# Performance work log

Hardware: AMD Instinct MI355X
Metric: run time of the kernel (lower is better)

Reference implementation:

```python
import jax, jax.numpy as jnp
import numpy as np

B, G, N = 32, 512, 512          # batch, group (POMO rollouts), problem size
EMB, H, DK = 128, 8, 16          # embedding_dim, head_num, qkv_dim (H*DK == EMB)
E, FH, K = 8, 512, 2             # num_experts, ff_hidden_dim, top-k
SQRT_EMB = 11.313708498984761    # sqrt(128), model_params['sqrt_embedding_dim']
CLIP = 10.0                      # logit_clipping


def setup_inputs() -> dict:
    key = jax.random.key(0)
    ks = jax.random.split(key, 22)
    s = 0.05
    d = {}
    d["pref"] = jax.random.uniform(ks[0], (2,), dtype=jnp.float32)
    d["graph"] = jax.random.normal(ks[1], (B, 1, EMB), dtype=jnp.float32)
    d["capacity"] = jax.random.uniform(ks[2], (B, G), dtype=jnp.float32)
    d["encoded_nodes"] = jax.random.normal(ks[3], (B, N, EMB), dtype=jnp.float32)
    d["ninf_mask"] = jnp.zeros((B, G, N), dtype=jnp.float32)
    # hyper-network MLP (note: original has NO activations between hyper_fc layers)
    d["fc1_w"] = jax.random.normal(ks[4], (256, 2)) * s
    d["fc1_b"] = jax.random.normal(ks[5], (256,)) * s
    d["fc2_w"] = jax.random.normal(ks[6], (256, 256)) * s
    d["fc2_b"] = jax.random.normal(ks[7], (256,)) * s
    d["fc3_w"] = jax.random.normal(ks[8], (8, 256)) * s
    d["fc3_b"] = jax.random.normal(ks[9], (8,)) * s
    # hyper heads producing the attention weight matrices (Linear(embd_dim=2, out), no bias)
    d["hWq"] = jax.random.normal(ks[10], ((1 + EMB) * H * DK, 2)) * 0.02
    d["hWk"] = jax.random.normal(ks[11], (EMB * H * DK, 2)) * 0.02
    d["hWv"] = jax.random.normal(ks[12], (EMB * H * DK, 2)) * 0.02
    d["hWc"] = jax.random.normal(ks[13], (EMB * H * DK, 2)) * 0.02
    # MoE combine layer: gating (token input + 8-dim pref embedding) and E expert MLPs
    d["gate_w"] = jax.random.normal(ks[14], (H * DK, E)) * s
    d["gate_pref_w"] = jax.random.normal(ks[15], (8, E)) * s
    d["e_w1"] = jax.random.normal(ks[16], (E, FH, H * DK)) * (1.0 / np.sqrt(H * DK))
    d["e_b1"] = jnp.zeros((E, FH), dtype=jnp.float32)
    d["e_w2"] = jax.random.normal(ks[17], (E, EMB, FH)) * (1.0 / np.sqrt(FH))
    d["e_b2"] = jnp.zeros((E, EMB), dtype=jnp.float32)
    d = {k2: v.astype(jnp.float32) for k2, v in d.items()}
    return d


def _heads(x):  # [B, n, H*DK] -> [B, H, n, DK]
    b, n, _ = x.shape
    return x.reshape(b, n, H, DK).transpose(0, 2, 1, 3)


def reference(pref, graph, capacity, encoded_nodes, ninf_mask,
              fc1_w, fc1_b, fc2_w, fc2_b, fc3_w, fc3_b,
              hWq, hWk, hWv, hWc,
              gate_w, gate_pref_w, e_w1, e_b1, e_w2, e_b2):
    # ---- assign(pref): hypernet generates attention weight matrices ----
    h = fc1_w @ pref + fc1_b
    h = fc2_w @ h + fc2_b
    mid = fc3_w @ h + fc3_b                      # [8] == mid_embd_pref
    Wq = (hWq @ mid[0:2]).reshape(H * DK, 1 + EMB)
    Wk = (hWk @ mid[2:4]).reshape(H * DK, EMB)
    Wv = (hWv @ mid[4:6]).reshape(H * DK, EMB)
    Wc = (hWc @ mid[6:8]).reshape(H * DK, EMB)
    # ---- set_kv ----
    k = _heads(encoded_nodes @ Wk.T)             # [B,H,N,DK]
    v = _heads(encoded_nodes @ Wv.T)
    # ---- forward ----
    inp = jnp.concatenate(
        [jnp.broadcast_to(graph, (B, G, EMB)), capacity[:, :, None]], axis=2)
    q = _heads(inp @ Wq.T)                       # [B,H,G,DK]
    score = jnp.einsum('bhgd,bhnd->bhgn', q, k) / jnp.sqrt(jnp.float32(DK))
    score = score + ninf_mask[:, None, :, :]
    attn = jax.nn.softmax(score, axis=3)
    out = jnp.einsum('bhgn,bhnd->bhgd', attn, v)
    out = out.transpose(0, 2, 1, 3).reshape(B, G, H * DK)   # [B,G,128]
    # ---- MoE combine (noisy top-k gating, deterministic at inference) ----
    logits = out @ gate_w + mid @ gate_pref_w    # [B,G,E]
    vals, idx = jax.lax.top_k(logits, K)
    gv = jax.nn.softmax(vals, axis=-1)           # softmax over selected k (T=1)
    gates = jnp.sum(jax.nn.one_hot(idx, E, dtype=out.dtype) * gv[..., None], axis=-2)
    hdn = jax.nn.relu(jnp.einsum('bgi,ehi->bgeh', out, e_w1) + e_b1)
    y = jnp.einsum('bgeh,eoh->bgeo', hdn, e_w2) + e_b2
    moe_out = jnp.einsum('bgeo,bge->bgo', y, gates)          # [B,G,EMB]
    # ---- combine + tanh-clipped masked softmax over nodes ----
    mh = moe_out @ Wc.T                           # [B,G,EMB]
    sc = jnp.einsum('bge,bne->bgn', mh, encoded_nodes) / SQRT_EMB
    probs = jax.nn.softmax(CLIP * jnp.tanh(sc) + ninf_mask, axis=2)
    return probs
```

## Files before the change

### kernel.cpp

```cpp
#include <hip/hip_runtime.h>


typedef __attribute__((ext_vector_type(8))) __bf16 bf16x8;
typedef __attribute__((ext_vector_type(4))) float f32x4;

static constexpr long OFF_MID   = 0;
static constexpr long OFF_PREFL = 8;
static constexpr long OFF_WL    = 16;
static constexpr long OFF_WKB   = 256;
static constexpr long OFF_WVB   = 8448;
static constexpr long OFF_WCB   = 16640;
static constexpr long OFF_QB    = 24832;
static constexpr long OFF_MFLAG = 28928;
static constexpr long OFF_CNT   = 33024;
static constexpr long OFF_TOK   = 33032;
static constexpr long OFF_WGT   = 164104;
static constexpr long OFF_AO    = 295176;
static constexpr long OFF_Y0    = 1343752;
static constexpr long OFF_Y1    = 2392328;
static constexpr long OFF_ENCB  = 3440904;

__device__ __forceinline__ unsigned f2bf(float x) {
  union { float f; unsigned u; } v; v.f = x;
  return ((v.u + 0x7FFFu + ((v.u >> 16) & 1u)) >> 16) & 0xFFFFu;
}
__device__ __forceinline__ float bflo(unsigned u) {
  union { unsigned u; float f; } v; v.u = u << 16; return v.f;
}
__device__ __forceinline__ float bfhi(unsigned u) {
  union { unsigned u; float f; } v; v.u = u & 0xFFFF0000u; return v.f;
}

__global__ __launch_bounds__(256)
void k_prep1(const float* __restrict__ pref, const float* __restrict__ fc1w,
             const float* __restrict__ fc1b, const float* __restrict__ fc2w,
             const float* __restrict__ fc2b, const float* __restrict__ fc3w,
             const float* __restrict__ fc3b, const float* __restrict__ gpw,
             const float* __restrict__ hWq, const float* __restrict__ mask,
             const float* __restrict__ ew1, const float* __restrict__ ew2,
             const float* __restrict__ enc,
             unsigned short* __restrict__ w1b, unsigned short* __restrict__ w2b,
             unsigned short* __restrict__ encb, float* __restrict__ ws) {
  const int bid = blockIdx.x;
  const int tid = threadIdx.x;
  if (bid == 0) {
    __shared__ float h1[256];
    __shared__ float h2[256];
    __shared__ float mid[8];
    const float p0 = pref[0], p1 = pref[1];
    h1[tid] = fc1w[2*tid]*p0 + fc1w[2*tid+1]*p1 + fc1b[tid];
    __syncthreads();
    float s = 0.f;
    for (int j = 0; j < 256; ++j) s = fmaf(fc2w[tid*256+j], h1[j], s);
    h2[tid] = s + fc2b[tid];
    __syncthreads();
    if (tid < 8) {
      float s2 = 0.f;
      for (int j = 0; j < 256; ++j) s2 = fmaf(fc3w[tid*256+j], h2[j], s2);
      mid[tid] = s2 + fc3b[tid];
    }
    __syncthreads();
    if (tid < 8) {
      ws[OFF_MID + tid] = mid[tid];
      float s3 = 0.f;
      for (int i = 0; i < 8; ++i) s3 = fmaf(mid[i], gpw[i*8 + tid], s3);
      ws[OFF_PREFL + tid] = s3;
      ((int*)(ws + OFF_CNT))[tid] = 0;
    }
    if (tid >= 16 && tid < 144) {
      const int o = tid - 16;
      ws[OFF_WL + o] = hWq[((long)o*129 + 128)*2]*mid[0]
                     + hWq[((long)o*129 + 128)*2 + 1]*mid[1];
    }
    return;
  }
  if (bid <= 3072) {
    const int i = (bid-1)*256 + tid;
    const float* src;
    unsigned short* dst;
    if (i < 131072)      { src = ew1 + (long)i*4;          dst = w1b + (long)i*4; }
    else if (i < 262144) { src = ew2 + (long)(i-131072)*4; dst = w2b + (long)(i-131072)*4; }
    else                 { src = enc + (long)(i-262144)*4; dst = encb + (long)(i-262144)*4; }
    const float4 v = *(const float4*)src;
    uint2 p;
    p.x = f2bf(v.x) | (f2bf(v.y) << 16);
    p.y = f2bf(v.z) | (f2bf(v.w) << 16);
    *(uint2*)dst = p;
    return;
  }
  __shared__ int fl[8];
  const int rowbase = (bid - 3073) * 8;
  const int r = tid >> 5, seg = tid & 31;
  if (tid < 8) fl[tid] = 0;
  __syncthreads();
  const float* mrow = mask + (long)(rowbase + r)*512 + seg*16;
  int nz = 0;
#pragma unroll
  for (int c = 0; c < 4; ++c) {
    const float4 v = *(const float4*)(mrow + c*4);
    nz |= (v.x != 0.f) | (v.y != 0.f) | (v.z != 0.f) | (v.w != 0.f);
  }
  if (nz) atomicOr(&fl[r], 1);
  __syncthreads();
  if (tid < 8) ((char*)(ws + OFF_MFLAG))[rowbase + tid] = (char)fl[tid];
}

__global__ __launch_bounds__(256)
void k_prep2(const float* __restrict__ graph,
             const float* __restrict__ hWq, const float* __restrict__ hWk,
             const float* __restrict__ hWv, const float* __restrict__ hWc,
             float* __restrict__ ws) {
  const int bid = blockIdx.x;
  const int tid = threadIdx.x;
  __shared__ float mid[8];
  __shared__ float g[2][128];
  if (tid < 8) mid[tid] = ws[OFF_MID + tid];
  __syncthreads();
  if (bid < 192) {
    const int i = bid*256 + tid;
    if (i < 16384) {
      ((unsigned short*)(ws + OFF_WKB))[i] =
          (unsigned short)f2bf(hWk[2*i]*mid[2] + hWk[2*i+1]*mid[3]);
    } else if (i < 32768) {
      const int j = i - 16384;
      ((unsigned short*)(ws + OFF_WVB))[j] =
          (unsigned short)f2bf(hWv[2*j]*mid[4] + hWv[2*j+1]*mid[5]);
    } else {
      const int j = i - 32768;
      ((unsigned short*)(ws + OFF_WCB))[j] =
          (unsigned short)f2bf(hWc[2*j]*mid[6] + hWc[2*j+1]*mid[7]);
    }
    return;
  }
  const int qb = bid - 192;
  const int b0 = qb*2;
  {
    const int bb = tid >> 7, ii = tid & 127;
    g[bb][ii] = graph[(b0+bb)*128 + ii];
  }
  __syncthreads();
  const float m0 = mid[0], m1 = mid[1];
  const int bb = tid >> 7, o = tid & 127;
  const float* hq = hWq + (long)o*129*2;
  float acc = 0.f;
  for (int i2 = 0; i2 < 128; ++i2) {
    const float w = hq[2*i2]*m0 + hq[2*i2+1]*m1;
    acc = fmaf(g[bb][i2], w, acc);
  }
  ws[OFF_QB + (b0+bb)*128 + o] = acc;
}

__device__ __forceinline__ bf16x8 ld_frag(const unsigned short* base, int row, int bytecol) {
  const int addr = row*256 + (bytecol ^ ((row & 7) << 4));
  return *(const bf16x8*)((const char*)base + addr);
}

__global__ __launch_bounds__(256)
void k_kv(const unsigned short* __restrict__ encb,
          const unsigned short* __restrict__ wkb,
          const unsigned short* __restrict__ wvb,
          unsigned short* __restrict__ Kb, unsigned short* __restrict__ Vtg) {
  __shared__ unsigned short Ws[128*128];
  __shared__ unsigned short Xs[64*128];
  const int tid = threadIdx.x;
  const int nbase = blockIdx.x * 64;
  const unsigned short* Wb = blockIdx.y ? wvb : wkb;
#pragma unroll
  for (int s = 0; s < 8; ++s) {
    const int id = tid + s*256;
    const int fr = id >> 4, c16 = id & 15;
    const uint4 v = *(const uint4*)(Wb + (long)fr*128 + c16*8);
    *(uint4*)((char*)Ws + fr*256 + ((c16*16) ^ ((fr & 7) << 4))) = v;
  }
#pragma unroll
  for (int s = 0; s < 4; ++s) {
    const int id = tid + s*256;
    const int r = id >> 4, c16 = id & 15;
    const uint4 v = *(const uint4*)(encb + (long)(nbase + r)*128 + c16*8);
    *(uint4*)((char*)Xs + r*256 + ((c16*16) ^ ((r & 7) << 4))) = v;
  }
  __syncthreads();
  const int w = tid >> 6, l = tid & 63, lq = l >> 4, lr = l & 15;
  f32x4 acc[2][4];
#pragma unroll
  for (int a = 0; a < 2; ++a)
#pragma unroll
    for (int m = 0; m < 4; ++m) acc[a][m] = (f32x4){0.f, 0.f, 0.f, 0.f};
#pragma unroll
  for (int ks = 0; ks < 4; ++ks) {
    const int bcol = ks*64 + lq*16;
    const bf16x8 a0 = ld_frag(Ws, (2*w  )*16 + lr, bcol);
    const bf16x8 a1 = ld_frag(Ws, (2*w+1)*16 + lr, bcol);
    const bf16x8 b0 = ld_frag(Xs, 0*16 + lr, bcol);
    const bf16x8 b1 = ld_frag(Xs, 1*16 + lr, bcol);
    const bf16x8 b2 = ld_frag(Xs, 2*16 + lr, bcol);
    const bf16x8 b3 = ld_frag(Xs, 3*16 + lr, bcol);
    acc[0][0] = __builtin_amdgcn_mfma_f32_16x16x32_bf16(a0, b0, acc[0][0], 0, 0, 0);
    acc[0][1] = __builtin_amdgcn_mfma_f32_16x16x32_bf16(a0, b1, acc[0][1], 0, 0, 0);
    acc[0][2] = __builtin_amdgcn_mfma_f32_16x16x32_bf16(a0, b2, acc[0][2], 0, 0, 0);
    acc[0][3] = __builtin_amdgcn_mfma_f32_16x16x32_bf16(a0, b3, acc[0][3], 0, 0, 0);
    acc[1][0] = __builtin_amdgcn_mfma_f32_16x16x32_bf16(a1, b0, acc[1][0], 0, 0, 0);
    acc[1][1] = __builtin_amdgcn_mfma_f32_16x16x32_bf16(a1, b1, acc[1][1], 0, 0, 0);
    acc[1][2] = __builtin_amdgcn_mfma_f32_16x16x32_bf16(a1, b2, acc[1][2], 0, 0, 0);
    acc[1][3] = __builtin_amdgcn_mfma_f32_16x16x32_bf16(a1, b3, acc[1][3], 0, 0, 0);
  }
  if (blockIdx.y == 0) {
#pragma unroll
    for (int obi = 0; obi < 2; ++obi) {
      const int o0 = (2*w + obi)*16 + lq*4;
#pragma unroll
      for (int mb = 0; mb < 4; ++mb) {
        const long n = nbase + mb*16 + lr;
        uint2 pp;
        pp.x = f2bf(acc[obi][mb][0]) | (f2bf(acc[obi][mb][1]) << 16);
        pp.y = f2bf(acc[obi][mb][2]) | (f2bf(acc[obi][mb][3]) << 16);
        *(uint2*)(Kb + n*128 + o0) = pp;
      }
    }
  } else {
    const int b = nbase >> 9;
    const int nn0 = nbase & 511;
#pragma unroll
    for (int obi = 0; obi < 2; ++obi) {
      const int o0 = (2*w + obi)*16 + lq*4;
#pragma unroll
      for (int mb = 0; mb < 4; ++mb) {
        const int nn = nn0 + mb*16 + lr;
#pragma unroll
        for (int j = 0; j < 4; ++j) {
          const int o = o0 + j;
          Vtg[(((long)b*8 + (o >> 4))*16 + (o & 15))*512 + nn] =
              (unsigned short)f2bf(acc[obi][mb][j]);
        }
      }
    }
  }
}

__global__ __launch_bounds__(512, 8)
void k_attn(const unsigned short* __restrict__ Kb,
            const unsigned short* __restrict__ Vtg,
            const float* __restrict__ ws, const float* __restrict__ cap,
            const float* __restrict__ mask, unsigned short* __restrict__ AOb) {
  const int bid = blockIdx.x;
  const int b = bid & 31, h = (bid >> 5) & 7, qh = bid >> 8;
  __shared__ unsigned short Kbf[512*24];
  __shared__ unsigned short Vt[16*536];
  __shared__ unsigned short Ps[8*16*40];
  const int tid = threadIdx.x;
#pragma unroll
  for (int it = 0; it < 2; ++it) {
    const int i = tid + it*512;
    const int n = i >> 1, hf = i & 1;
    const uint4 kv = *(const uint4*)(Kb + (long)(b*512 + n)*128 + h*16 + hf*8);
    *(uint4*)(Kbf + n*24 + hf*8) = kv;
    const int d = i >> 6, c = i & 63;
    const uint4 vv = *(const uint4*)(Vtg + ((long)(b*8 + h)*16 + d)*512 + c*8);
    *(uint4*)(Vt + d*536 + c*8) = vv;
  }
  const int w = tid >> 6, l = tid & 63;
  const int lq = l >> 4, lr = l & 15;
  const int grow = qh*128 + w*16 + lr;
  bf16x8 qf;
  {
    union { uint4 u; bf16x8 v; } cv;
    cv.u = make_uint4(0u, 0u, 0u, 0u);
    if (lq < 2) {
      const float* qbp = ws + OFF_QB + b*128 + h*16 + lq*8;
      const float* wlp = ws + OFF_WL + h*16 + lq*8;
      const float cp = cap[b*512 + grow];
      float qv[8];
#pragma unroll
      for (int j = 0; j < 8; ++j) qv[j] = (qbp[j] + cp*wlp[j]) * 0.25f;
      cv.u.x = f2bf(qv[0]) | (f2bf(qv[1]) << 16);
      cv.u.y = f2bf(qv[2]) | (f2bf(qv[3]) << 16);
      cv.u.z = f2bf(qv[4]) | (f2bf(qv[5]) << 16);
      cv.u.w = f2bf(qv[6]) | (f2bf(qv[7]) << 16);
    }
    qf = cv.v;
  }
  const int mf = ((const char*)(ws + OFF_MFLAG))[b*512 + grow];
  const bool usemask = __any(mf != 0);
  unsigned short* Pw = Ps + w*16*40;
  const int psw = (lr & 3) << 3;
  __syncthreads();
  float lsum = 0.f;
  f32x4 oaccA = {0.f, 0.f, 0.f, 0.f};
  f32x4 oaccB = {0.f, 0.f, 0.f, 0.f};
  const float* mrow = mask + ((long)(b*512 + grow))*512 + lq*4;
#pragma unroll 2
  for (int qc = 0; qc < 16; ++qc) {
    const int n0 = qc*32;
    f32x4 s[2];
#pragma unroll
    for (int nb = 0; nb < 2; ++nb) {
      bf16x8 kf;
      {
        union { uint4 u; bf16x8 v; } cv;
        cv.u = make_uint4(0u, 0u, 0u, 0u);
        if (lq < 2) cv.u = *(const uint4*)(Kbf + (n0 + nb*16 + lr)*24 + lq*8);
        kf = cv.v;
      }
      s[nb] = __builtin_amdgcn_mfma_f32_16x16x32_bf16(
          kf, qf, (f32x4){0.f, 0.f, 0.f, 0.f}, 0, 0, 0);
      if (usemask) {
        const float4 mk = *(const float4*)(mrow + n0 + nb*16);
        s[nb][0] += mk.x; s[nb][1] += mk.y; s[nb][2] += mk.z; s[nb][3] += mk.w;
      }
    }
#pragma unroll
    for (int nb = 0; nb < 2; ++nb) {
      const float e0 = __expf(s[nb][0]);
      const float e1 = __expf(s[nb][1]);
      const float e2 = __expf(s[nb][2]);
      const float e3 = __expf(s[nb][3]);
      lsum += (e0 + e1) + (e2 + e3);
      uint2 pp;
      asm("v_cvt_pk_bf16_f32 %0, %1, %2" : "=v"(pp.x) : "v"(e0), "v"(e1));
      asm("v_cvt_pk_bf16_f32 %0, %1, %2" : "=v"(pp.y) : "v"(e2), "v"(e3));
      *(uint2*)(Pw + lr*40 + ((nb*16 + lq*4) ^ psw)) = pp;
    }
    const bf16x8 va = *(const bf16x8*)(Vt + lr*536 + n0 + lq*8);
    const bf16x8 pb = *(const bf16x8*)(Pw + lr*40 + (lq*8 ^ psw));
    if (qc & 1) oaccB = __builtin_amdgcn_mfma_f32_16x16x32_bf16(va, pb, oaccB, 0, 0, 0);
    else        oaccA = __builtin_amdgcn_mfma_f32_16x16x32_bf16(va, pb, oaccA, 0, 0, 0);
  }
  lsum += __shfl_xor(lsum, 16);
  lsum += __shfl_xor(lsum, 32);
  const float inv = 1.f / lsum;
  uint2 op;
  op.x = f2bf((oaccA[0]+oaccB[0])*inv) | (f2bf((oaccA[1]+oaccB[1])*inv) << 16);
  op.y = f2bf((oaccA[2]+oaccB[2])*inv) | (f2bf((oaccA[3]+oaccB[3])*inv) << 16);
  *(uint2*)(AOb + (long)(b*512 + grow)*128 + h*16 + lq*4) = op;
}

__global__ __launch_bounds__(256)
void k_gate(const unsigned short* __restrict__ AOb, const float* __restrict__ gw,
            float* __restrict__ ws) {
  const int tid = threadIdx.x;
  const int t = blockIdx.x*256 + tid;
  const unsigned short* x = AOb + (long)t*128;
  float lg[8];
  {
    const float* pl = ws + OFF_PREFL;
#pragma unroll
    for (int e = 0; e < 8; ++e) lg[e] = pl[e];
  }
  for (int i = 0; i < 128; i += 8) {
    const uint4 xv = *(const uint4*)(x + i);
    float xf[8];
    xf[0] = bflo(xv.x); xf[1] = bfhi(xv.x);
    xf[2] = bflo(xv.y); xf[3] = bfhi(xv.y);
    xf[4] = bflo(xv.z); xf[5] = bfhi(xv.z);
    xf[6] = bflo(xv.w); xf[7] = bfhi(xv.w);
#pragma unroll
    for (int u = 0; u < 8; ++u) {
      const float xi = xf[u];
      const float4 ga = *(const float4*)(gw + (i+u)*8);
      const float4 gb = *(const float4*)(gw + (i+u)*8 + 4);
      lg[0] = fmaf(xi, ga.x, lg[0]); lg[1] = fmaf(xi, ga.y, lg[1]);
      lg[2] = fmaf(xi, ga.z, lg[2]); lg[3] = fmaf(xi, ga.w, lg[3]);
      lg[4] = fmaf(xi, gb.x, lg[4]); lg[5] = fmaf(xi, gb.y, lg[5]);
      lg[6] = fmaf(xi, gb.z, lg[6]); lg[7] = fmaf(xi, gb.w, lg[7]);
    }
  }
  int i0 = 0; float v0 = lg[0];
#pragma unroll
  for (int e = 1; e < 8; ++e) if (lg[e] > v0) { v0 = lg[e]; i0 = e; }
  int i1 = -1; float v1 = -1e30f;
#pragma unroll
  for (int e = 0; e < 8; ++e) if (e != i0 && lg[e] > v1) { v1 = lg[e]; i1 = e; }
  const float e1 = __expf(v1 - v0);
  const float w0 = 1.f / (1.f + e1);
  const float w1 = 1.f - w0;
  __shared__ int bcnt[8];
  __shared__ int gbase[8];
  if (tid < 8) bcnt[tid] = 0;
  __syncthreads();
  const int p0 = atomicAdd(&bcnt[i0], 1);
  const int p1 = atomicAdd(&bcnt[i1], 1);
  __syncthreads();
  if (tid < 8) {
    int* cnt = (int*)(ws + OFF_CNT);
    gbase[tid] = (bcnt[tid] > 0) ? atomicAdd(&cnt[tid], bcnt[tid]) : 0;
  }
  __syncthreads();
  int* tokp = (int*)(ws + OFF_TOK);
  float* wgtp = ws + OFF_WGT;
  const int s0 = gbase[i0] + p0;
  tokp[i0*16384 + s0] = t;
  wgtp[i0*16384 + s0] = w0;
  const int s1 = gbase[i1] + p1;
  tokp[i1*16384 + s1] = t | (1 << 30);
  wgtp[i1*16384 + s1] = w1;
}

__global__ __launch_bounds__(256)
void k_moe(const unsigned short* __restrict__ AOb,
           const unsigned short* __restrict__ w1b,
           const unsigned short* __restrict__ w2b,
           const float* __restrict__ eb1, const float* __restrict__ eb2,
           float* __restrict__ ws,
           unsigned short* __restrict__ Y0b, unsigned short* __restrict__ Y1b) {
  const int e = blockIdx.y;
  const int ce = ((const int*)(ws + OFF_CNT))[e];
  const int base = blockIdx.x * 64;
  if (base >= ce) return;
  const int nt = min(64, ce - base);

  __shared__ unsigned short Xs[64*128];
  __shared__ unsigned short Wts[128*128];
  __shared__ unsigned short Hs[64*128];
  __shared__ float seb1[512];
  __shared__ float seb2[128];
  __shared__ int   stok[64];
  __shared__ float swgt[64];

  const int tid = threadIdx.x;
  if (tid < 64) {
    if (tid < nt) {
      stok[tid] = ((const int*)(ws + OFF_TOK))[e*16384 + base + tid];
      swgt[tid] = (ws + OFF_WGT)[e*16384 + base + tid];
    } else { stok[tid] = -1; swgt[tid] = 0.f; }
  }
  for (int i = tid; i < 512; i += 256) seb1[i] = eb1[e*512 + i];
  if (tid < 128) seb2[tid] = eb2[e*128 + tid];
  __syncthreads();

#pragma unroll
  for (int r4 = 0; r4 < 4; ++r4) {
    const int id = tid + r4*256;
    const int r = id >> 4, c16 = id & 15;
    const int pk = stok[r];
    uint4 v = make_uint4(0u, 0u, 0u, 0u);
    if (pk >= 0) v = *(const uint4*)(AOb + (long)(pk & 0x3FFFFFFF)*128 + c16*8);
    *(uint4*)((char*)Xs + r*256 + ((c16*16) ^ ((r & 7) << 4))) = v;
  }

  const int w  = tid >> 6;
  const int l  = tid & 63;
  const int lq = l >> 4;
  const int lr = l & 15;

  f32x4 yacc[2][4];
#pragma unroll
  for (int a = 0; a < 2; ++a)
#pragma unroll
    for (int m = 0; m < 4; ++m) yacc[a][m] = (f32x4){0.f, 0.f, 0.f, 0.f};

  for (int fc = 0; fc < 4; ++fc) {
    __syncthreads();
    {
      const long wb = (long)(e*512 + fc*128) * 128;
#pragma unroll
      for (int s = 0; s < 8; ++s) {
        const int id = tid + s*256;
        const int fr = id >> 4, c16 = id & 15;
        const uint4 v = *(const uint4*)(w1b + wb + (long)fr*128 + c16*8);
        *(uint4*)((char*)Wts + fr*256 + ((c16*16) ^ ((fr & 7) << 4))) = v;
      }
    }
    __syncthreads();
    f32x4 hacc[2][4];
#pragma unroll
    for (int a = 0; a < 2; ++a)
#pragma unroll
      for (int m = 0; m < 4; ++m) hacc[a][m] = (f32x4){0.f, 0.f, 0.f, 0.f};
#pragma unroll
    for (int ks = 0; ks < 4; ++ks) {
      const int bcol = ks*64 + lq*16;
      const bf16x8 a0 = ld_frag(Wts, (2*w  )*16 + lr, bcol);
      const bf16x8 a1 = ld_frag(Wts, (2*w+1)*16 + lr, bcol);
      const bf16x8 b0 = ld_frag(Xs,  0*16 + lr, bcol);
      const bf16x8 b1 = ld_frag(Xs,  1*16 + lr, bcol);
      const bf16x8 b2 = ld_frag(Xs,  2*16 + lr, bcol);
      const bf16x8 b3 = ld_frag(Xs,  3*16 + lr, bcol);
      hacc[0][0] = __builtin_amdgcn_mfma_f32_16x16x32_bf16(a0, b0, hacc[0][0], 0, 0, 0);
      hacc[0][1] = __builtin_amdgcn_mfma_f32_16x16x32_bf16(a0, b1, hacc[0][1], 0, 0, 0);
      hacc[0][2] = __builtin_amdgcn_mfma_f32_16x16x32_bf16(a0, b2, hacc[0][2], 0, 0, 0);
      hacc[0][3] = __builtin_amdgcn_mfma_f32_16x16x32_bf16(a0, b3, hacc[0][3], 0, 0, 0);
      hacc[1][0] = __builtin_amdgcn_mfma_f32_16x16x32_bf16(a1, b0, hacc[1][0], 0, 0, 0);
      hacc[1][1] = __builtin_amdgcn_mfma_f32_16x16x32_bf16(a1, b1, hacc[1][1], 0, 0, 0);
      hacc[1][2] = __builtin_amdgcn_mfma_f32_16x16x32_bf16(a1, b2, hacc[1][2], 0, 0, 0);
      hacc[1][3] = __builtin_amdgcn_mfma_f32_16x16x32_bf16(a1, b3, hacc[1][3], 0, 0, 0);
    }
    __syncthreads();
#pragma unroll
    for (int fbi = 0; fbi < 2; ++fbi) {
      const int fb = (2*w + fbi)*16 + lq*4;
      const float4 bia = *(const float4*)&seb1[fc*128 + fb];
#pragma unroll
      for (int mb = 0; mb < 4; ++mb) {
        const int m = mb*16 + lr;
        const float h0 = fmaxf(hacc[fbi][mb][0] + bia.x, 0.f);
        const float h1 = fmaxf(hacc[fbi][mb][1] + bia.y, 0.f);
        const float h2 = fmaxf(hacc[fbi][mb][2] + bia.z, 0.f);
        const float h3 = fmaxf(hacc[fbi][mb][3] + bia.w, 0.f);
        uint2 p;
        p.x = f2bf(h0) | (f2bf(h1) << 16);
        p.y = f2bf(h2) | (f2bf(h3) << 16);
        const int bc = (fb*2) ^ ((m & 7) << 4);
        *(uint2*)((char*)Hs + m*256 + bc) = p;
      }
    }
    {
      const long wb = (long)(e*128) * 512 + fc*128;
#pragma unroll
      for (int s = 0; s < 8; ++s) {
        const int id = tid + s*256;
        const int orr = id >> 4, c16 = id & 15;
        const uint4 v = *(const uint4*)(w2b + wb + (long)orr*512 + c16*8);
        *(uint4*)((char*)Wts + orr*256 + ((c16*16) ^ ((orr & 7) << 4))) = v;
      }
    }
    __syncthreads();
#pragma unroll
    for (int ks = 0; ks < 4; ++ks) {
      const int bcol = ks*64 + lq*16;
      const bf16x8 a0 = ld_frag(Wts, (2*w  )*16 + lr, bcol);
      const bf16x8 a1 = ld_frag(Wts, (2*w+1)*16 + lr, bcol);
      const bf16x8 b0 = ld_frag(Hs,  0*16 + lr, bcol);
      const bf16x8 b1 = ld_frag(Hs,  1*16 + lr, bcol);
      const bf16x8 b2 = ld_frag(Hs,  2*16 + lr, bcol);
      const bf16x8 b3 = ld_frag(Hs,  3*16 + lr, bcol);
      yacc[0][0] = __builtin_amdgcn_mfma_f32_16x16x32_bf16(a0, b0, yacc[0][0], 0, 0, 0);
      yacc[0][1] = __builtin_amdgcn_mfma_f32_16x16x32_bf16(a0, b1, yacc[0][1], 0, 0, 0);
      yacc[0][2] = __builtin_amdgcn_mfma_f32_16x16x32_bf16(a0, b2, yacc[0][2], 0, 0, 0);
      yacc[0][3] = __builtin_amdgcn_mfma_f32_16x16x32_bf16(a0, b3, yacc[0][3], 0, 0, 0);
      yacc[1][0] = __builtin_amdgcn_mfma_f32_16x16x32_bf16(a1, b0, yacc[1][0], 0, 0, 0);
      yacc[1][1] = __builtin_amdgcn_mfma_f32_16x16x32_bf16(a1, b1, yacc[1][1], 0, 0, 0);
      yacc[1][2] = __builtin_amdgcn_mfma_f32_16x16x32_bf16(a1, b2, yacc[1][2], 0, 0, 0);
      yacc[1][3] = __builtin_amdgcn_mfma_f32_16x16x32_bf16(a1, b3, yacc[1][3], 0, 0, 0);
    }
  }
#pragma unroll
  for (int obi = 0; obi < 2; ++obi) {
    const int ob = (2*w + obi)*16 + lq*4;
    const float4 b2 = *(const float4*)&seb2[ob];
#pragma unroll
    for (int mb = 0; mb < 4; ++mb) {
      const int tl = mb*16 + lr;
      if (tl < nt) {
        const int pk = stok[tl];
        const int tk = pk & 0x3FFFFFFF;
        const float wgt = swgt[tl];
        unsigned short* Yp = ((pk >> 30) ? Y1b : Y0b) + (long)tk*128 + ob;
        uint2 p;
        p.x = f2bf((yacc[obi][mb][0] + b2.x) * wgt)
            | (f2bf((yacc[obi][mb][1] + b2.y) * wgt) << 16);
        p.y = f2bf((yacc[obi][mb][2] + b2.z) * wgt)
            | (f2bf((yacc[obi][mb][3] + b2.w) * wgt) << 16);
        *(uint2*)Yp = p;
      }
    }
  }
}

__global__ __launch_bounds__(512)
void k_gemm2f(const unsigned short* __restrict__ Y0b,
              const unsigned short* __restrict__ Y1b,
              const unsigned short* __restrict__ wcb,
              const unsigned short* __restrict__ encb,
              const float* __restrict__ mask,
              const char* __restrict__ mflag,
              float* __restrict__ out) {
  const int bid = blockIdx.x;
  const int b = bid & 31, rt = bid >> 5;
  __shared__ unsigned short Amh[64*128];
  __shared__ unsigned short Bch[512*32];
  __shared__ float red[64][9];
  __shared__ char sfl[64];
  const int tid = threadIdx.x;
  const int w = tid >> 6, l = tid & 63, lq = l >> 4, lr = l & 15;
  const long rowbase = (long)b*512 + rt*64;
#pragma unroll
  for (int s = 0; s < 2; ++s) {
    const int id = tid + s*512;
    const int r = id >> 4, c16 = id & 15;
    const long yb = (rowbase + r)*128 + c16*8;
    const uint4 a = *(const uint4*)(Y0b + yb);
    const uint4 c = *(const uint4*)(Y1b + yb);
    uint4 p;
    p.x = f2bf(bflo(a.x)+bflo(c.x)) | (f2bf(bfhi(a.x)+bfhi(c.x)) << 16);
    p.y = f2bf(bflo(a.y)+bflo(c.y)) | (f2bf(bfhi(a.y)+bfhi(c.y)) << 16);
    p.z = f2bf(bflo(a.z)+bflo(c.z)) | (f2bf(bfhi(a.z)+bfhi(c.z)) << 16);
    p.w = f2bf(bflo(a.w)+bflo(c.w)) | (f2bf(bfhi(a.w)+bfhi(c.w)) << 16);
    *(uint4*)((char*)Amh + r*256 + ((c16*16) ^ ((r & 7) << 4))) = p;
  }
#pragma unroll
  for (int s = 0; s < 4; ++s) {
    const int id = tid + s*512;
    const int fr = id >> 4, c16 = id & 15;
    const uint4 v = *(const uint4*)(wcb + (long)fr*128 + c16*8);
    *(uint4*)((char*)Bch + fr*256 + ((c16*16) ^ ((fr & 7) << 4))) = v;
  }
  if (tid < 64) sfl[tid] = mflag[rowbase + tid];
  __syncthreads();
  {
    f32x4 macc[4];
#pragma unroll
    for (int m = 0; m < 4; ++m) macc[m] = (f32x4){0.f, 0.f, 0.f, 0.f};
#pragma unroll
    for (int ks = 0; ks < 4; ++ks) {
      const int bcol = ks*64 + lq*16;
      const bf16x8 a0 = ld_frag(Bch, w*16 + lr, bcol);
      const bf16x8 b0 = ld_frag(Amh, 0*16 + lr, bcol);
      const bf16x8 b1 = ld_frag(Amh, 1*16 + lr, bcol);
      const bf16x8 b2 = ld_frag(Amh, 2*16 + lr, bcol);
      const bf16x8 b3 = ld_frag(Amh, 3*16 + lr, bcol);
      macc[0] = __builtin_amdgcn_mfma_f32_16x16x32_bf16(a0, b0, macc[0], 0, 0, 0);
      macc[1] = __builtin_amdgcn_mfma_f32_16x16x32_bf16(a0, b1, macc[1], 0, 0, 0);
      macc[2] = __builtin_amdgcn_mfma_f32_16x16x32_bf16(a0, b2, macc[2], 0, 0, 0);
      macc[3] = __builtin_amdgcn_mfma_f32_16x16x32_bf16(a0, b3, macc[3], 0, 0, 0);
    }
    __syncthreads();
    const int o0 = w*16 + lq*4;
#pragma unroll
    for (int mb = 0; mb < 4; ++mb) {
      const int m = mb*16 + lr;
      uint2 p;
      p.x = f2bf(macc[mb][0]) | (f2bf(macc[mb][1]) << 16);
      p.y = f2bf(macc[mb][2]) | (f2bf(macc[mb][3]) << 16);
      *(uint2*)((char*)Amh + m*256 + ((o0*2) ^ ((m & 7) << 4))) = p;
    }
  }
  f32x4 acc[4][4];
#pragma unroll
  for (int mi = 0; mi < 4; ++mi)
#pragma unroll
    for (int ni = 0; ni < 4; ++ni) acc[mi][ni] = (f32x4){0.f, 0.f, 0.f, 0.f};
  for (int kc = 0; kc < 4; ++kc) {
    __syncthreads();
#pragma unroll
    for (int s = 0; s < 4; ++s) {
      const int id = tid + s*512;
      const int n = id >> 2, sl = id & 3;
      const uint4 v = *(const uint4*)(encb + ((long)b*512 + n)*128 + kc*32 + sl*8);
      *(uint4*)((char*)Bch + n*64 + ((sl*16) ^ ((n & 3) << 4))) = v;
    }
    __syncthreads();
    bf16x8 af[4], bfr[4];
#pragma unroll
    for (int mi = 0; mi < 4; ++mi) {
      const int r = mi*16 + lr;
      af[mi] = *(const bf16x8*)((const char*)Amh + r*256 + ((kc*64 + lq*16) ^ ((r & 7) << 4)));
    }
#pragma unroll
    for (int ni = 0; ni < 4; ++ni) {
      const int n = w*64 + ni*16 + lr;
      bfr[ni] = *(const bf16x8*)((const char*)Bch + n*64 + ((lq*16) ^ ((n & 3) << 4)));
    }
#pragma unroll
    for (int mi = 0; mi < 4; ++mi)
#pragma unroll
      for (int ni = 0; ni < 4; ++ni)
        acc[mi][ni] = __builtin_amdgcn_mfma_f32_16x16x32_bf16(af[mi], bfr[ni], acc[mi][ni], 0, 0, 0);
  }
  const float ISC = 1.f/11.313708498984761f;
  float rsum[4][4];
#pragma unroll
  for (int mi = 0; mi < 4; ++mi)
#pragma unroll
    for (int j = 0; j < 4; ++j) rsum[mi][j] = 0.f;
#pragma unroll
  for (int mi = 0; mi < 4; ++mi) {
#pragma unroll
    for (int j = 0; j < 4; ++j) {
      const int rl = mi*16 + lq*4 + j;
      const bool um = sfl[rl] != 0;
      const float* mrow = mask + (rowbase + rl)*512 + w*64 + lr;
#pragma unroll
      for (int ni = 0; ni < 4; ++ni) {
        const float sc = acc[mi][ni][j] * ISC;
        const float mv = um ? mrow[ni*16] : 0.f;
        const float li = 10.f*tanhf(sc) + mv;
        const float e = __expf(li - 10.f);
        acc[mi][ni][j] = e;
        rsum[mi][j] += e;
      }
    }
  }
#pragma unroll
  for (int mi = 0; mi < 4; ++mi)
#pragma unroll
    for (int j = 0; j < 4; ++j) {
#pragma unroll
      for (int o = 1; o < 16; o <<= 1) rsum[mi][j] += __shfl_xor(rsum[mi][j], o);
    }
  if (lr == 0) {
#pragma unroll
    for (int mi = 0; mi < 4; ++mi)
#pragma unroll
      for (int j = 0; j < 4; ++j) red[mi*16 + lq*4 + j][w] = rsum[mi][j];
  }
  __syncthreads();
  if (tid < 64) {
    float s = 0.f;
#pragma unroll
    for (int wv = 0; wv < 8; ++wv) s += red[tid][wv];
    red[tid][8] = 1.f / s;
  }
  __syncthreads();
#pragma unroll
  for (int mi = 0; mi < 4; ++mi) {
#pragma unroll
    for (int j = 0; j < 4; ++j) {
      const int rl = mi*16 + lq*4 + j;
      const float inv = red[rl][8];
      float* orow = out + (rowbase + rl)*512 + w*64 + lr;
#pragma unroll
      for (int ni = 0; ni < 4; ++ni) orow[ni*16] = acc[mi][ni][j] * inv;
    }
  }
}

extern "C" void kernel_launch(void* const* d_in, const int* in_sizes, int n_in,
                              void* d_out, int out_size, void* d_ws, size_t ws_size,
                              hipStream_t stream) {
  (void)in_sizes; (void)n_in; (void)out_size; (void)ws_size;
  const float* pref  = (const float*)d_in[0];
  const float* graph = (const float*)d_in[1];
  const float* cap   = (const float*)d_in[2];
  const float* enc   = (const float*)d_in[3];
  const float* mask  = (const float*)d_in[4];
  const float* fc1w  = (const float*)d_in[5];
  const float* fc1b  = (const float*)d_in[6];
  const float* fc2w  = (const float*)d_in[7];
  const float* fc2b  = (const float*)d_in[8];
  const float* fc3w  = (const float*)d_in[9];
  const float* fc3b  = (const float*)d_in[10];
  const float* hWq   = (const float*)d_in[11];
  const float* hWk   = (const float*)d_in[12];
  const float* hWv   = (const float*)d_in[13];
  const float* hWc   = (const float*)d_in[14];
  const float* gw    = (const float*)d_in[15];
  const float* gpw   = (const float*)d_in[16];
  const float* ew1   = (const float*)d_in[17];
  const float* eb1   = (const float*)d_in[18];
  const float* ew2   = (const float*)d_in[19];
  const float* eb2   = (const float*)d_in[20];
  float* ws  = (float*)d_ws;
  float* out = (float*)d_out;
  unsigned short* Kbuf = (unsigned short*)out;
  unsigned short* Vtg  = (unsigned short*)(out + 1048576);
  unsigned short* ew1b = (unsigned short*)(out + 4194304);
  unsigned short* ew2b = (unsigned short*)(out + 4456448);
  unsigned short* AOb  = (unsigned short*)(ws + OFF_AO);
  unsigned short* Y0b  = (unsigned short*)(ws + OFF_Y0);
  unsigned short* Y1b  = (unsigned short*)(ws + OFF_Y1);
  unsigned short* encb = (unsigned short*)(ws + OFF_ENCB);
  unsigned short* wkb  = (unsigned short*)(ws + OFF_WKB);
  unsigned short* wvb  = (unsigned short*)(ws + OFF_WVB);
  unsigned short* wcb  = (unsigned short*)(ws + OFF_WCB);
  const char* mflag = (const char*)(ws + OFF_MFLAG);

  k_prep1<<<5121, 256, 0, stream>>>(pref, fc1w, fc1b, fc2w, fc2b, fc3w, fc3b,
                                    gpw, hWq, mask, ew1, ew2, enc,
                                    ew1b, ew2b, encb, ws);
  k_prep2<<<208, 256, 0, stream>>>(graph, hWq, hWk, hWv, hWc, ws);
  k_kv<<<dim3(256, 2), 256, 0, stream>>>(encb, wkb, wvb, Kbuf, Vtg);
  k_attn<<<1024, 512, 0, stream>>>(Kbuf, Vtg, ws, cap, mask, AOb);
  k_gate<<<64, 256, 0, stream>>>(AOb, gw, ws);
  k_moe<<<dim3(256, 8), 256, 0, stream>>>(AOb, ew1b, ew2b, eb1, eb2, ws, Y0b, Y1b);
  k_gemm2f<<<256, 512, 0, stream>>>(Y0b, Y1b, wcb, encb, mask, mflag, out);
}
```

Baseline: 112.4 us.

## Double MoE token tile to 128 with 512 threads; use fast tanh in softmax

The MoE expert kernel now processes 128 tokens per block with 8 waves instead of 64 tokens with 4 waves, so each expert weight chunk staged into shared memory is reused across twice as many tokens. Each wave now owns one 16-row weight slice against all 8 token sub-tiles. The aim is to halve redundant weight loads and the number of blocks. Separately, tanhf in the final softmax is replaced by an exp/rcp formulation to cut transcendental cost, at a small accuracy cost. The larger tile raises shared memory use, which may lower occupancy, and experts with few tokens waste more of each tile.

```diff
diff --git a/kernel.cpp b/kernel.cpp
--- a/kernel.cpp
+++ b/kernel.cpp
@@ -395,7 +395,7 @@
   wgtp[i1*16384 + s1] = w1;
 }
 
-__global__ __launch_bounds__(256)
+__global__ __launch_bounds__(512)
 void k_moe(const unsigned short* __restrict__ AOb,
            const unsigned short* __restrict__ w1b,
            const unsigned short* __restrict__ w2b,
@@ -404,32 +404,32 @@
            unsigned short* __restrict__ Y0b, unsigned short* __restrict__ Y1b) {
   const int e = blockIdx.y;
   const int ce = ((const int*)(ws + OFF_CNT))[e];
-  const int base = blockIdx.x * 64;
+  const int base = blockIdx.x * 128;
   if (base >= ce) return;
-  const int nt = min(64, ce - base);
-
-  __shared__ unsigned short Xs[64*128];
+  const int nt = min(128, ce - base);
+
+  __shared__ unsigned short Xs[128*128];
   __shared__ unsigned short Wts[128*128];
-  __shared__ unsigned short Hs[64*128];
+  __shared__ unsigned short Hs[128*128];
   __shared__ float seb1[512];
   __shared__ float seb2[128];
-  __shared__ int   stok[64];
-  __shared__ float swgt[64];
+  __shared__ int   stok[128];
+  __shared__ float swgt[128];
 
   const int tid = threadIdx.x;
-  if (tid < 64) {
+  if (tid < 128) {
     if (tid < nt) {
       stok[tid] = ((const int*)(ws + OFF_TOK))[e*16384 + base + tid];
       swgt[tid] = (ws + OFF_WGT)[e*16384 + base + tid];
     } else { stok[tid] = -1; swgt[tid] = 0.f; }
   }
-  for (int i = tid; i < 512; i += 256) seb1[i] = eb1[e*512 + i];
-  if (tid < 128) seb2[tid] = eb2[e*128 + tid];
+  if (tid >= 128 && tid < 256) seb2[tid-128] = eb2[e*128 + tid-128];
+  seb1[tid] = eb1[e*512 + tid];
   __syncthreads();
 
 #pragma unroll
   for (int r4 = 0; r4 < 4; ++r4) {
-    const int id = tid + r4*256;
+    const int id = tid + r4*512;
     const int r = id >> 4, c16 = id & 15;
     const int pk = stok[r];
     uint4 v = make_uint4(0u, 0u, 0u, 0u);
@@ -442,60 +442,47 @@
   const int lq = l >> 4;
   const int lr = l & 15;
 
-  f32x4 yacc[2][4];
-#pragma unroll
-  for (int a = 0; a < 2; ++a)
-#pragma unroll
-    for (int m = 0; m < 4; ++m) yacc[a][m] = (f32x4){0.f, 0.f, 0.f, 0.f};
+  f32x4 yacc[8];
+#pragma unroll
+  for (int m = 0; m < 8; ++m) yacc[m] = (f32x4){0.f, 0.f, 0.f, 0.f};
 
   for (int fc = 0; fc < 4; ++fc) {
     __syncthreads();
     {
       const long wb = (long)(e*512 + fc*128) * 128;
 #pragma unroll
-      for (int s = 0; s < 8; ++s) {
-        const int id = tid + s*256;
+      for (int s = 0; s < 4; ++s) {
+        const int id = tid + s*512;
         const int fr = id >> 4, c16 = id & 15;
         const uint4 v = *(const uint4*)(w1b + wb + (long)fr*128 + c16*8);
         *(uint4*)((char*)Wts + fr*256 + ((c16*16) ^ ((fr & 7) << 4))) = v;
       }
     }
     __syncthreads();
-    f32x4 hacc[2][4];
-#pragma unroll
-    for (int a = 0; a < 2; ++a)
-#pragma unroll
-      for (int m = 0; m < 4; ++m) hacc[a][m] = (f32x4){0.f, 0.f, 0.f, 0.f};
+    f32x4 hacc[8];
+#pragma unroll
+    for (int m = 0; m < 8; ++m) hacc[m] = (f32x4){0.f, 0.f, 0.f, 0.f};
 #pragma unroll
     for (int ks = 0; ks < 4; ++ks) {
       const int bcol = ks*64 + lq*16;
-      const bf16x8 a0 = ld_frag(Wts, (2*w  )*16 + lr, bcol);
-      const bf16x8 a1 = ld_frag(Wts, (2*w+1)*16 + lr, bcol);
-      const bf16x8 b0 = ld_frag(Xs,  0*16 + lr, bcol);
-      const bf16x8 b1 = ld_frag(Xs,  1*16 + lr, bcol);
-      const bf16x8 b2 = ld_frag(Xs,  2*16 + lr, bcol);
-      const bf16x8 b3 = ld_frag(Xs,  3*16 + lr, bcol);
-      hacc[0][0] = __builtin_amdgcn_mfma_f32_16x16x32_bf16(a0, b0, hacc[0][0], 0, 0, 0);
-      hacc[0][1] = __builtin_amdgcn_mfma_f32_16x16x32_bf16(a0, b1, hacc[0][1], 0, 0, 0);
-      hacc[0][2] = __builtin_amdgcn_mfma_f32_16x16x32_bf16(a0, b2, hacc[0][2], 0, 0, 0);
-      hacc[0][3] = __builtin_amdgcn_mfma_f32_16x16x32_bf16(a0, b3, hacc[0][3], 0, 0, 0);
-      hacc[1][0] = __builtin_amdgcn_mfma_f32_16x16x32_bf16(a1, b0, hacc[1][0], 0, 0, 0);
-      hacc[1][1] = __builtin_amdgcn_mfma_f32_16x16x32_bf16(a1, b1, hacc[1][1], 0, 0, 0);
-      hacc[1][2] = __builtin_amdgcn_mfma_f32_16x16x32_bf16(a1, b2, hacc[1][2], 0, 0, 0);
-      hacc[1][3] = __builtin_amdgcn_mfma_f32_16x16x32_bf16(a1, b3, hacc[1][3], 0, 0, 0);
-    }
-    __syncthreads();
-#pragma unroll
-    for (int fbi = 0; fbi < 2; ++fbi) {
-      const int fb = (2*w + fbi)*16 + lq*4;
+      const bf16x8 a0 = ld_frag(Wts, w*16 + lr, bcol);
+#pragma unroll
+      for (int mb = 0; mb < 8; ++mb) {
+        const bf16x8 bm = ld_frag(Xs, mb*16 + lr, bcol);
+        hacc[mb] = __builtin_amdgcn_mfma_f32_16x16x32_bf16(a0, bm, hacc[mb], 0, 0, 0);
+      }
+    }
+    __syncthreads();
+    {
+      const int fb = w*16 + lq*4;
       const float4 bia = *(const float4*)&seb1[fc*128 + fb];
 #pragma unroll
-      for (int mb = 0; mb < 4; ++mb) {
+      for (int mb = 0; mb < 8; ++mb) {
         const int m = mb*16 + lr;
-        const float h0 = fmaxf(hacc[fbi][mb][0] + bia.x, 0.f);
-        const float h1 = fmaxf(hacc[fbi][mb][1] + bia.y, 0.f);
-        const float h2 = fmaxf(hacc[fbi][mb][2] + bia.z, 0.f);
-        const float h3 = fmaxf(hacc[fbi][mb][3] + bia.w, 0.f);
+        const float h0 = fmaxf(hacc[mb][0] + bia.x, 0.f);
+        const float h1 = fmaxf(hacc[mb][1] + bia.y, 0.f);
+        const float h2 = fmaxf(hacc[mb][2] + bia.z, 0.f);
+        const float h3 = fmaxf(hacc[mb][3] + bia.w, 0.f);
         uint2 p;
         p.x = f2bf(h0) | (f2bf(h1) << 16);
         p.y = f2bf(h2) | (f2bf(h3) << 16);
@@ -506,8 +493,8 @@
     {
       const long wb = (long)(e*128) * 512 + fc*128;
 #pragma unroll
-      for (int s = 0; s < 8; ++s) {
-        const int id = tid + s*256;
+      for (int s = 0; s < 4; ++s) {
+        const int id = tid + s*512;
         const int orr = id >> 4, c16 = id & 15;
         const uint4 v = *(const uint4*)(w2b + wb + (long)orr*512 + c16*8);
         *(uint4*)((char*)Wts + orr*256 + ((c16*16) ^ ((orr & 7) << 4))) = v;
@@ -517,28 +504,19 @@
 #pragma unroll
     for (int ks = 0; ks < 4; ++ks) {
       const int bcol = ks*64 + lq*16;
-      const bf16x8 a0 = ld_frag(Wts, (2*w  )*16 + lr, bcol);
-      const bf16x8 a1 = ld_frag(Wts, (2*w+1)*16 + lr, bcol);
-      const bf16x8 b0 = ld_frag(Hs,  0*16 + lr, bcol);
-      const bf16x8 b1 = ld_frag(Hs,  1*16 + lr, bcol);
-      const bf16x8 b2 = ld_frag(Hs,  2*16 + lr, bcol);
-      const bf16x8 b3 = ld_frag(Hs,  3*16 + lr, bcol);
-      yacc[0][0] = __builtin_amdgcn_mfma_f32_16x16x32_bf16(a0, b0, yacc[0][0], 0, 0, 0);
-      yacc[0][1] = __builtin_amdgcn_mfma_f32_16x16x32_bf16(a0, b1, yacc[0][1], 0, 0, 0);
-      yacc[0][2] = __builtin_amdgcn_mfma_f32_16x16x32_bf16(a0, b2, yacc[0][2], 0, 0, 0);
-      yacc[0][3] = __builtin_amdgcn_mfma_f32_16x16x32_bf16(a0, b3, yacc[0][3], 0, 0, 0);
-      yacc[1][0] = __builtin_amdgcn_mfma_f32_16x16x32_bf16(a1, b0, yacc[1][0], 0, 0, 0);
-      yacc[1][1] = __builtin_amdgcn_mfma_f32_16x16x32_bf16(a1, b1, yacc[1][1], 0, 0, 0);
-      yacc[1][2] = __builtin_amdgcn_mfma_f32_16x16x32_bf16(a1, b2, yacc[1][2], 0, 0, 0);
-      yacc[1][3] = __builtin_amdgcn_mfma_f32_16x16x32_bf16(a1, b3, yacc[1][3], 0, 0, 0);
-    }
-  }
-#pragma unroll
-  for (int obi = 0; obi < 2; ++obi) {
-    const int ob = (2*w + obi)*16 + lq*4;
+      const bf16x8 a0 = ld_frag(Wts, w*16 + lr, bcol);
+#pragma unroll
+      for (int mb = 0; mb < 8; ++mb) {
+        const bf16x8 bm = ld_frag(Hs, mb*16 + lr, bcol);
+        yacc[mb] = __builtin_amdgcn_mfma_f32_16x16x32_bf16(a0, bm, yacc[mb], 0, 0, 0);
+      }
+    }
+  }
+  {
+    const int ob = w*16 + lq*4;
     const float4 b2 = *(const float4*)&seb2[ob];
 #pragma unroll
-    for (int mb = 0; mb < 4; ++mb) {
+    for (int mb = 0; mb < 8; ++mb) {
       const int tl = mb*16 + lr;
       if (tl < nt) {
         const int pk = stok[tl];
@@ -546,10 +524,10 @@
         const float wgt = swgt[tl];
         unsigned short* Yp = ((pk >> 30) ? Y1b : Y0b) + (long)tk*128 + ob;
         uint2 p;
-        p.x = f2bf((yacc[obi][mb][0] + b2.x) * wgt)
-            | (f2bf((yacc[obi][mb][1] + b2.y) * wgt) << 16);
-        p.y = f2bf((yacc[obi][mb][2] + b2.z) * wgt)
-            | (f2bf((yacc[obi][mb][3] + b2.w) * wgt) << 16);
+        p.x = f2bf((yacc[mb][0] + b2.x) * wgt)
+            | (f2bf((yacc[mb][1] + b2.y) * wgt) << 16);
+        p.y = f2bf((yacc[mb][2] + b2.z) * wgt)
+            | (f2bf((yacc[mb][3] + b2.w) * wgt) << 16);
         *(uint2*)Yp = p;
       }
     }
@@ -672,8 +650,10 @@
 #pragma unroll
       for (int ni = 0; ni < 4; ++ni) {
         const float sc = acc[mi][ni][j] * ISC;
+        const float t = __expf(-2.f * fabsf(sc));
+        const float th = (1.f - t) * __builtin_amdgcn_rcpf(1.f + t);
         const float mv = um ? mrow[ni*16] : 0.f;
-        const float li = 10.f*tanhf(sc) + mv;
+        const float li = copysignf(th, sc)*10.f + mv;
         const float e = __expf(li - 10.f);
         acc[mi][ni][j] = e;
         rsum[mi][j] += e;
@@ -761,6 +741,6 @@
   k_kv<<<dim3(256, 2), 256, 0, stream>>>(encb, wkb, wvb, Kbuf, Vtg);
   k_attn<<<1024, 512, 0, stream>>>(Kbuf, Vtg, ws, cap, mask, AOb);
   k_gate<<<64, 256, 0, stream>>>(AOb, gw, ws);
-  k_moe<<<dim3(256, 8), 256, 0, stream>>>(AOb, ew1b, ew2b, eb1, eb2, ws, Y0b, Y1b);
+  k_moe<<<dim3(128, 8), 512, 0, stream>>>(AOb, ew1b, ew2b, eb1, eb2, ws, Y0b, Y1b);
   k_gemm2f<<<256, 512, 0, stream>>>(Y0b, Y1b, wcb, encb, mask, mflag, out);
 }
```

Result: slower. 126.9 us (+12.9%).
